# Kernel tuning notes

Hardware: AMD Instinct MI355X
Metric: run time of the kernel (lower is better)

Reference implementation:

```python
import jax, jax.numpy as jnp
import numpy as np

B, N, C, HF, WF = 32, 1000, 64, 12, 20
Y_DISC = 72
D = C * HF  # 768: flattened anchor feature dim (channels x fv height)


def setup_inputs() -> dict:
    key = jax.random.key(0)
    ks = jax.random.split(key, 8)
    feature_volumes = jax.random.normal(ks[0], (B, C, HF, WF), jnp.float32)
    # Anchor gather indices: channel index, row index, per-anchor x along the anchor line
    z_idx = jnp.broadcast_to(jnp.arange(C, dtype=jnp.int32)[None, :, None], (N, C, HF))
    y_idx = jnp.broadcast_to(jnp.arange(HF, dtype=jnp.int32)[None, None, :], (N, C, HF))
    x_line = jax.random.randint(ks[1], (N, 1, HF), 0, WF, dtype=jnp.int32)
    x_idx = jnp.broadcast_to(x_line, (N, C, HF))
    invalid_mask = jnp.broadcast_to(jax.random.bernoulli(ks[2], 0.2, (N, 1, HF)), (N, C, HF))
    attn_w = jax.random.normal(ks[3], (D, N - 1), jnp.float32) * 0.02
    attn_b = jnp.zeros((N - 1,), jnp.float32)
    cls_w = jax.random.normal(ks[4], (2 * D, 2), jnp.float32) * 0.02
    cls_b = jnp.zeros((2,), jnp.float32)
    reg_w = jax.random.normal(ks[5], (2 * D, Y_DISC + 1), jnp.float32) * 0.02
    reg_b = jnp.zeros((Y_DISC + 1,), jnp.float32)
    anchors_image = jax.random.normal(ks[6], (N, 5 + Y_DISC), jnp.float32)
    return {
        'feature_volumes': feature_volumes,
        'attn_w': attn_w, 'attn_b': attn_b,
        'cls_w': cls_w, 'cls_b': cls_b,
        'reg_w': reg_w, 'reg_b': reg_b,
        'anchors_image': anchors_image,
        'z_idx': z_idx, 'y_idx': y_idx, 'x_idx': x_idx,
        'invalid_mask': invalid_mask,
    }


def reference(feature_volumes, attn_w, attn_b, cls_w, cls_b, reg_w, reg_b,
              anchors_image, z_idx, y_idx, x_idx, invalid_mask):
    b = feature_volumes.shape[0]
    n = z_idx.shape[0]
    # __cut_anchor_features: gather (B, N, C, HF) rois, zero invalid entries
    rois = feature_volumes[:, z_idx, y_idx, x_idx]          # (B, N, C, HF)
    rois = jnp.where(invalid_mask[None], 0.0, rois)
    feat = rois.reshape(b, n, D)                            # (B, N, D)
    # attention layer: Linear(D -> N-1) + softmax over the N-1 dim
    scores = jax.nn.softmax(feat @ attn_w + attn_b, axis=-1)  # (B, N, N-1)
    # scatter scores into the off-diagonal of an NxN matrix (diagonal = 0)
    rows = jnp.arange(n)
    k = jnp.arange(n - 1)
    col_idx = jnp.where(k[None, :] < rows[:, None], k[None, :], k[None, :] + 1)  # (N, N-1)
    attn_mat = jnp.zeros((b, n, n), feat.dtype).at[:, rows[:, None], col_idx].set(scores)
    # bmm: attention-weighted sum of anchor features
    att_feat = jnp.einsum('bij,bjd->bid', attn_mat, feat)   # (B, N, D)
    cat = jnp.concatenate([att_feat, feat], axis=-1)        # (B, N, 2D)
    cls_logits = cat @ cls_w + cls_b                        # (B, N, 2)
    reg = cat @ reg_w + reg_b                               # (B, N, 73)
    anchors = jnp.broadcast_to(anchors_image[None], (b, n, 5 + Y_DISC))
    # proposals: [:2]=cls, [2:4]=anchor, [4:]=anchor+reg
    return jnp.concatenate([cls_logits, anchors[:, :, 2:4], anchors[:, :, 4:] + reg], axis=-1)
```

## Files before the change

### kernel.cpp

```cpp
#include <hip/hip_runtime.h>
#include <hip/hip_bf16.h>

typedef _Float16 f16;
typedef _Float16 f16x4 __attribute__((ext_vector_type(4)));
typedef _Float16 f16x8 __attribute__((ext_vector_type(8)));
typedef float    f32x4 __attribute__((ext_vector_type(4)));

static __device__ __forceinline__ float bf2f(__hip_bfloat16 x) { return __bfloat162float(x); }
static __device__ __forceinline__ float ldf(const void* p, long i, int f32flag) {
    return f32flag ? ((const float*)p)[i] : bf2f(((const __hip_bfloat16*)p)[i]);
}
static __device__ __forceinline__ void stf(void* p, long i, int f32flag, float v) {
    if (f32flag) ((float*)p)[i] = v;
    else ((__hip_bfloat16*)p)[i] = __float2bfloat16(v);
}
static __device__ __forceinline__ void gl2lds16(const f16* g, f16* l) {
    __builtin_amdgcn_global_load_lds(
        (const __attribute__((address_space(1))) unsigned int*)(const void*)g,
        (__attribute__((address_space(3))) unsigned int*)(void*)l, 16, 0, 0);
}

#define OFF_LOGITS 0L
#define SZ_LOGITS  (32000L * 1024 * 2)
#define OFF_FEAT   (OFF_LOGITS + SZ_LOGITS)
#define SZ_FEAT    (32000L * 768 * 2)
#define OFF_ATTF   (OFF_FEAT + SZ_FEAT)
#define SZ_ATTF    (32000L * 768 * 2)
#define OFF_AWT    (OFF_ATTF + SZ_ATTF)
#define SZ_AWT     (1024L * 768 * 2)
#define OFF_WCT    (OFF_AWT + SZ_AWT)
#define SZ_WCT     (128L * 1536 * 2)
#define OFF_BIAS   (OFF_WCT + SZ_WCT)
#define OFF_AB     (OFF_BIAS + 512)
#define OFF_FLAG   (OFF_AB + 4096)
#define OFF_FEATT  (OFF_FLAG + 64)
#define SZ_FEATT   (32L * 768 * 1024 * 2)
#define NEED_A     (OFF_FEATT + SZ_FEATT)

__global__ void detect_kernel(const unsigned int* __restrict__ fv,
                              const unsigned int* __restrict__ m,
                              int mwords, int* __restrict__ flags)
{
    __shared__ int cnt, bits;
    int t = threadIdx.x;
    if (t == 0) { cnt = 0; bits = 0; }
    __syncthreads();
    int c = 0;
    for (int k = t; k < 2048; k += 256) {
        unsigned int w = fv[k];
        unsigned int h0 = w & 0xffffu, h1 = w >> 16;
        unsigned int e0 = (h0 >> 7) & 0xffu, e1 = (h1 >> 7) & 0xffu;
        c += (h0 == 0u || (e0 >= 100u && e0 <= 135u)) ? 1 : 0;
        c += (h1 == 0u || (e1 >= 100u && e1 <= 135u)) ? 1 : 0;
    }
    atomicAdd(&cnt, c);
    int lb = 0;
    for (int k = t; k < mwords; k += 256) {
        unsigned int w = m[k];
        if (w > 1u) lb |= 1;
        if ((k & 1) && w != 0u) lb |= 2;
        unsigned int lo = w & 0xffffu, hi = w >> 16;
        if (!((lo == 0u || lo == 0x3f80u) && (hi == 0u || hi == 0x3f80u))) lb |= 4;
        if (lo == 0x3f80u) lb |= 8;
    }
    if (lb) atomicOr(&bits, lb);
    __syncthreads();
    if (t == 0) {
        int b = bits, f;
        if (!(b & 1))      f = (b & 2) ? 0 : 3;
        else if (!(b & 4)) f = (b & 8) ? 2 : 4;
        else               f = 1;
        flags[0] = f;
        flags[1] = (cnt < 3900) ? 1 : 0;
    }
}

__global__ __launch_bounds__(256) void front_kernel(
    const void* __restrict__ fv, const int* __restrict__ x_idx,
    const void* __restrict__ maskp, const int* __restrict__ flags,
    int xstride, int mstride, f16* __restrict__ feat,
    const void* __restrict__ attn_w,
    const void* __restrict__ cls_w, const void* __restrict__ cls_b,
    const void* __restrict__ reg_w, const void* __restrict__ reg_b,
    const void* __restrict__ attn_b,
    f16* __restrict__ awT, f16* __restrict__ wcT,
    float* __restrict__ biasc, float* __restrict__ abf32)
{
    int bid = blockIdx.x;
    int t = threadIdx.x;
    int isf = flags[1], fm = flags[0];
    if (bid < 512) {
        __shared__ f16 sfv[15360];
        __shared__ int sx[756];
        __shared__ unsigned char sm[756];
        int b = bid >> 4, n0 = (bid & 15) * 63;
        int rows = min(63, 1000 - n0);
        if (isf) {
            const float4* src = (const float4*)fv + (long)b * 3840;
            for (int k = t; k < 3840; k += 256) {
                float4 v = src[k];
                f16x4 h; h[0] = (f16)v.x; h[1] = (f16)v.y; h[2] = (f16)v.z; h[3] = (f16)v.w;
                *(f16x4*)&sfv[k * 4] = h;
            }
        } else {
            const uint4* src = (const uint4*)fv + (long)b * 1920;
            for (int k = t; k < 1920; k += 256) {
                uint4 v = src[k];
                unsigned int wv[4] = {v.x, v.y, v.z, v.w};
                f16x8 h;
                #pragma unroll
                for (int j = 0; j < 4; j++) {
                    h[2 * j]     = (f16)__uint_as_float((wv[j] & 0xffffu) << 16);
                    h[2 * j + 1] = (f16)__uint_as_float(wv[j] & 0xffff0000u);
                }
                *(f16x8*)&sfv[k * 8] = h;
            }
        }
        for (int k = t; k < rows * 12; k += 256) {
            int n = k / 12, h = k - n * 12;
            sx[k] = x_idx[(long)(n0 + n) * xstride + h];
            long mb = (long)(n0 + n) * mstride + h;
            int mv;
            if (fm == 0)      mv = ((const int*)maskp)[mb] != 0;
            else if (fm == 1) mv = ((const unsigned char*)maskp)[mb] != 0;
            else if (fm == 2) mv = ((const unsigned short*)maskp)[mb] != 0;
            else if (fm == 3) mv = ((const int*)maskp)[mb * 2] != 0;
            else              mv = ((const unsigned int*)maskp)[mb] != 0;
            sm[k] = (unsigned char)mv;
        }
        __syncthreads();
        for (int q = t; q < rows * 192; q += 256) {
            int n = q / 192, r = q - n * 192;
            int e0 = r * 4;
            f16x4 v;
            #pragma unroll
            for (int j = 0; j < 4; j++) {
                int e = e0 + j;
                int h = e % 12;
                int kk = n * 12 + h;
                v[j] = sm[kk] ? (f16)0.f : sfv[e * 20 + sx[kk]];
            }
            *(f16x4*)(feat + ((long)(b * 1000 + n0 + n)) * 768 + e0) = v;
        }
    } else if (bid < 1280) {
        __shared__ f16 tile[32][33];
        int tid = bid - 512;
        int c0 = (tid % 32) * 32, r0 = (tid / 32) * 32;
        int tx = t & 31, ty = t >> 5;
        #pragma unroll
        for (int i = ty; i < 32; i += 8) {
            int r = r0 + i, c = c0 + tx;
            float v = 0.f;
            if (r < 768 && c < 999) v = ldf(attn_w, (long)r * 999 + c, isf);
            tile[i][tx] = (f16)v;
        }
        __syncthreads();
        #pragma unroll
        for (int i = ty; i < 32; i += 8) {
            int oc = c0 + i, orw = r0 + tx;
            awT[(long)oc * 768 + orw] = tile[tx][i];
        }
    } else {
        int idx = (bid - 1280) * 256 + t;
        if (idx < 128 * 1536) {
            int c = idx / 1536, k = idx - c * 1536;
            float v = 0.f;
            if (c < 2)       v = ldf(cls_w, (long)k * 2 + c, isf);
            else if (c < 75) v = ldf(reg_w, (long)k * 73 + (c - 2), isf);
            wcT[idx] = (f16)v;
        }
        if (idx < 75)
            biasc[idx] = (idx < 2) ? ldf(cls_b, idx, isf) : ldf(reg_b, idx - 2, isf);
        if (idx < 1024)
            abf32[idx] = (idx < 999) ? ldf(attn_b, idx, isf) : 0.f;
    }
}

__global__ __launch_bounds__(256) void transp_kernel(
    const f16* __restrict__ feat, f16* __restrict__ featT)
{
    __shared__ f16 tile[64][68];
    int bid = blockIdx.x;
    int bz = bid / 192;
    int rq = bid - bz * 192;
    int by = rq & 15, bx = rq >> 4;
    int r0 = by * 64, c0 = bx * 64;
    int t = threadIdx.x;
    int tr = t >> 4, tc = (t & 15) * 4;
    const f16* src = feat + (long)bz * 768000;
    #pragma unroll
    for (int ii = 0; ii < 4; ii++) {
        int r = r0 + ii * 16 + tr;
        f16x4 v = {(f16)0.f, (f16)0.f, (f16)0.f, (f16)0.f};
        if (r < 1000) v = *(const f16x4*)(src + (long)r * 768 + c0 + tc);
        *(f16x4*)&tile[ii * 16 + tr][tc] = v;
    }
    __syncthreads();
    f16* dst = featT + (long)bz * 786432;
    #pragma unroll
    for (int ii = 0; ii < 4; ii++) {
        int d = ii * 16 + tr;
        f16x4 v;
        #pragma unroll
        for (int j = 0; j < 4; j++) v[j] = tile[tc + j][d];
        *(f16x4*)(dst + (long)(c0 + d) * 1024 + r0 + tc) = v;
    }
}

__global__ __launch_bounds__(256) void post_kernel(
    f16* __restrict__ buf, const float* __restrict__ abf32)
{
    int bid = blockIdx.x;
    int t = threadIdx.x;
    int i = bid % 1000, b = bid / 1000;
    f16* row = buf + ((long)(b * 1000 + i)) * 1024;
    __shared__ float red[8];
    __shared__ float epv[256];
    int k0 = t * 4;
    f16x4 rv = *(const f16x4*)(row + k0);
    float4 ab = *(const float4*)(abf32 + k0);
    float abv[4] = {ab.x, ab.y, ab.z, ab.w};
    float v[4];
    float lmax = -3.4e38f;
    #pragma unroll
    for (int j = 0; j < 4; j++) {
        int k = k0 + j;
        float x = (k < 999) ? (float)rv[j] + abv[j] : -3.4e38f;
        v[j] = x;
        lmax = fmaxf(lmax, x);
    }
    #pragma unroll
    for (int o = 32; o > 0; o >>= 1) lmax = fmaxf(lmax, __shfl_down(lmax, o, 64));
    if ((t & 63) == 0) red[t >> 6] = lmax;
    __syncthreads();
    float gmax = fmaxf(fmaxf(red[0], red[1]), fmaxf(red[2], red[3]));
    float e[4];
    float lsum = 0.f;
    #pragma unroll
    for (int j = 0; j < 4; j++) {
        int k = k0 + j;
        float x = (k < 999) ? __expf(v[j] - gmax) : 0.f;
        e[j] = x;
        lsum += x;
    }
    epv[t] = e[3];
    #pragma unroll
    for (int o = 32; o > 0; o >>= 1) lsum += __shfl_down(lsum, o, 64);
    if ((t & 63) == 0) red[4 + (t >> 6)] = lsum;
    __syncthreads();
    float inv = 1.f / (red[4] + red[5] + red[6] + red[7]);
    f16x4 outv;
    if (k0 >= 1000) {
        #pragma unroll
        for (int j = 0; j < 4; j++) outv[j] = (f16)0.f;
    } else if (k0 + 3 < i) {
        #pragma unroll
        for (int j = 0; j < 4; j++) outv[j] = (f16)(e[j] * inv);
    } else if (k0 > i) {
        float ep = epv[t - 1];
        outv[0] = (f16)(ep * inv);
        #pragma unroll
        for (int j = 1; j < 4; j++) outv[j] = (f16)(e[j - 1] * inv);
    } else {
        #pragma unroll
        for (int j = 0; j < 4; j++) {
            int p = k0 + j;
            float s = (p == i) ? 0.f : ((p < i) ? e[j] : e[j - 1 < 0 ? 0 : j - 1]);
            if (p > i) s = e[j - 1];
            outv[j] = (f16)(s * inv);
        }
    }
    *(f16x4*)(row + k0) = outv;
}

#define SB8   __builtin_amdgcn_sched_barrier(0)
#define BAR8  __builtin_amdgcn_s_barrier()
#define LGKM0 do { asm volatile("s_waitcnt lgkmcnt(0)" ::: "memory"); __builtin_amdgcn_sched_barrier(0); } while (0)
#define VM4   asm volatile("s_waitcnt vmcnt(4)" ::: "memory")

__global__ __launch_bounds__(512, 2) void gemm8p_kernel(
    const f16* __restrict__ A, int lda,
    const f16* __restrict__ Bt, int ldb,
    f16* __restrict__ C, int ldc,
    int M, int MT, int NT, int KT,
    long sA, long sB, long sC)
{
    __shared__ __align__(16) f16 As[2][16384];
    __shared__ __align__(16) f16 Bs[2][16384];
    int t = threadIdx.x;
    int nwg = gridDim.x;
    int orig = blockIdx.x;
    int xcd = orig & 7, lin = orig >> 3;
    int q8 = nwg >> 3, r8 = nwg & 7;
    int wgid = (xcd < r8 ? xcd * (q8 + 1) : r8 * (q8 + 1) + (xcd - r8) * q8) + lin;
    int per_b = MT * NT;
    int bz = wgid / per_b;
    int rem = wgid - bz * per_b;
    int mt = rem / NT, nt = rem - mt * NT;
    int m0 = mt * 256, n0 = nt * 256;
    A  += (long)bz * sA;
    Bt += (long)bz * sB;
    C  += (long)bz * sC;
    int w = t >> 6, lane = t & 63;
    int wm = (w >> 2) * 128, wn = (w & 3) * 64;
    int lr = lane & 15, lq = lane >> 4;
    int row0 = t >> 3, slot = t & 7;
    int csw = slot ^ (row0 & 7);

    f32x4 acc[8][4];
    const f32x4 z4 = {0.f, 0.f, 0.f, 0.f};
    #pragma unroll
    for (int i = 0; i < 8; i++)
        #pragma unroll
        for (int j = 0; j < 4; j++) acc[i][j] = z4;

    f16x8 a_[2][2], b_[4][2];

#define STAGE_A8(kt, h, buf) do { \
    int ktc = (kt) < KT ? (kt) : KT - 1; \
    const f16* gp = A + (long)(m0 + (h) * 128 + row0) * lda + ktc * 64 + csw * 8; \
    gl2lds16(gp,                  &As[buf][(h) * 8192 + w * 512]); \
    gl2lds16(gp + 64 * (long)lda, &As[buf][(h) * 8192 + 4096 + w * 512]); \
} while (0)
#define STAGE_B8(kt, h, buf) do { \
    int ktc = (kt) < KT ? (kt) : KT - 1; \
    const f16* gp = Bt + (long)(n0 + (h) * 128 + row0) * ldb + ktc * 64 + csw * 8; \
    gl2lds16(gp,                  &Bs[buf][(h) * 8192 + w * 512]); \
    gl2lds16(gp + 64 * (long)ldb, &Bs[buf][(h) * 8192 + 4096 + w * 512]); \
} while (0)
#define RD_B8(buf) { \
    _Pragma("unroll") for (int n = 0; n < 4; n++) { \
        int r = wn + n * 16 + lr; int rb = r * 64; int x7 = r & 7; \
        _Pragma("unroll") for (int ks = 0; ks < 2; ks++) { \
            int cc = (lq + ks * 4) ^ x7; \
            b_[n][ks] = *(const f16x8*)&Bs[buf][rb + cc * 8]; } } }
#define RD_A8(q, buf) { \
    _Pragma("unroll") for (int m2 = 0; m2 < 2; m2++) { \
        int r = wm + ((q) * 2 + m2) * 16 + lr; int rb = r * 64; int x7 = r & 7; \
        _Pragma("unroll") for (int ks = 0; ks < 2; ks++) { \
            int cc = (lq + ks * 4) ^ x7; \
            a_[m2][ks] = *(const f16x8*)&As[buf][rb + cc * 8]; } } }
#define MFMA16(q) { \
    __builtin_amdgcn_s_setprio(1); \
    _Pragma("unroll") for (int ks = 0; ks < 2; ks++) \
    _Pragma("unroll") for (int m2 = 0; m2 < 2; m2++) \
    _Pragma("unroll") for (int n = 0; n < 4; n++) \
        acc[(q) * 2 + m2][n] = __builtin_amdgcn_mfma_f32_16x16x32_f16( \
            a_[m2][ks], b_[n][ks], acc[(q) * 2 + m2][n], 0, 0, 0); \
    __builtin_amdgcn_s_setprio(0); }

    STAGE_B8(0, 0, 0); STAGE_B8(0, 1, 0);
    STAGE_A8(0, 0, 0); STAGE_A8(0, 1, 0);
    STAGE_B8(1, 0, 1); STAGE_B8(1, 1, 1);
    VM4;
    BAR8;

    int NIT = KT >> 1;
    for (int it = 0; it < NIT; it++) {
        int t0 = 2 * it, t1 = t0 + 1;
        SB8; RD_B8(0); RD_A8(0, 0); STAGE_A8(t1, 0, 1);
        BAR8; LGKM0; MFMA16(0); BAR8;
        SB8; RD_A8(1, 0); STAGE_A8(t1, 1, 1);
        BAR8; LGKM0; MFMA16(1); BAR8;
        SB8; RD_A8(2, 0); STAGE_B8(t0 + 2, 0, 0);
        BAR8; LGKM0; MFMA16(2); BAR8;
        SB8; RD_A8(3, 0); STAGE_B8(t0 + 2, 1, 0);
        BAR8; LGKM0; MFMA16(3); VM4; BAR8;
        SB8; RD_B8(1); RD_A8(0, 1); STAGE_A8(t0 + 2, 0, 0);
        BAR8; LGKM0; MFMA16(0); BAR8;
        SB8; RD_A8(1, 1); STAGE_A8(t0 + 2, 1, 0);
        BAR8; LGKM0; MFMA16(1); BAR8;
        SB8; RD_A8(2, 1); STAGE_B8(t1 + 2, 0, 1);
        BAR8; LGKM0; MFMA16(2); BAR8;
        SB8; RD_A8(3, 1); STAGE_B8(t1 + 2, 1, 1);
        BAR8; LGKM0; MFMA16(3); VM4; BAR8;
    }

    #pragma unroll
    for (int m = 0; m < 8; m++)
        #pragma unroll
        for (int n = 0; n < 4; n++)
            #pragma unroll
            for (int r = 0; r < 4; r++) {
                int gm = m0 + wm + m * 16 + lq * 4 + r;
                int gn = n0 + wn + n * 16 + lr;
                if (gm < M) C[(long)gm * ldc + gn] = (f16)acc[m][n][r];
            }
#undef STAGE_A8
#undef STAGE_B8
#undef RD_B8
#undef RD_A8
#undef MFMA16
}

enum { OUT_F16 = 0, OUT_FINAL = 1 };

template<int MODE, bool CAT, bool BKM, int TM, int TN, int BK, int SWZ, bool BG>
__global__ __launch_bounds__(256, 2) void gemm_kernel(
    const f16* __restrict__ A, const f16* __restrict__ A2, int lda,
    const f16* __restrict__ Bt, int ldb,
    void* __restrict__ Cout, int ldc,
    int M, int Nc, int K,
    long sA, long sB, long sC,
    const float* __restrict__ bias, const void* __restrict__ anchors,
    const int* __restrict__ flags)
{
    int t = threadIdx.x;
    int bx, by, bz;
    if constexpr (SWZ == 2) {
        int bid = blockIdx.x;
        int xcd = bid & 7, s = bid >> 3;
        int g = xcd + 8 * (s >> 2);
        if (g >= (M + TM - 1) / TM) return;
        by = g; bx = s & 3; bz = 0;
    } else if constexpr (SWZ == 3) {
        int bid = blockIdx.x;
        int xcd = bid & 7, s = bid >> 3;
        bz = xcd * 4 + s / 24;
        int wv = s % 24;
        by = wv / 3; bx = wv - by * 3;
    } else { bx = blockIdx.x; by = blockIdx.y; bz = blockIdx.z; }

    int m0 = by * TM, n0 = bx * TN;
    int z = bz;
    A  += (long)z * sA;
    if (CAT) A2 += (long)z * sA;
    Bt += (long)z * sB;
    int w = t >> 6, lane = t & 63;
    constexpr int NJ = (TM == 128 && TN == 256) ? 8 : ((TN == 256) ? 4 : ((TM == 128) ? 4 : 2));
    int wm = (TM == 128) ? (w & 1) * 64 : 0;
    int wn;
    if constexpr (TM == 128 && TN == 256) wn = (w >> 1) * 128;
    else if constexpr (TN == 256)         wn = w * 64;
    else if constexpr (TM == 128)         wn = (w >> 1) * 64;
    else                                  wn = w * 32;

    int lr = lane & 15, lq = lane >> 4;

    const f32x4 zero4 = {0.f, 0.f, 0.f, 0.f};
    f32x4 acc[4][NJ];
    #pragma unroll
    for (int i = 0; i < 4; i++)
        #pragma unroll
        for (int j = 0; j < NJ; j++) acc[i][j] = zero4;

    if constexpr (BG) {
        constexpr int CH  = BK / 8;
        constexpr int AI  = TM * BK / 2048;
        constexpr int RPO = 2048 / BK;
        __shared__ __align__(16) f16 As[TM * BK];
        int row0 = t / CH, slot = t % CH;
        int csw = slot ^ (row0 & (CH - 1));
        long aoffB = (long)(m0 + row0) * lda + csw * 8;
        for (int k0 = 0; k0 < K; k0 += BK) {
            const f16* Ak = A; int kk = k0;
            if (CAT && k0 >= 768) { Ak = A2; kk = k0 - 768; }
            __syncthreads();
            #pragma unroll
            for (int i = 0; i < AI; i++)
                gl2lds16(Ak + aoffB + (long)(i * RPO) * lda + kk, &As[i * 2048 + w * 512]);
            f16x8 ball[BK / 32][NJ];
            #pragma unroll
            for (int ks = 0; ks < BK / 32; ks++)
                #pragma unroll
                for (int j = 0; j < NJ; j++) {
                    int r = wn + j * 16 + lr;
                    ball[ks][j] = *(const f16x8*)(Bt + (long)r * ldb + k0 + (ks * 4 + lq) * 8);
                }
            __syncthreads();
            #pragma unroll
            for (int ks = 0; ks < BK / 32; ks++) {
                f16x8 af[4];
                #pragma unroll
                for (int i = 0; i < 4; i++) {
                    int r = wm + i * 16 + lr;
                    int cc = (lq + ks * 4) ^ (r & (CH - 1));
                    af[i] = *(const f16x8*)&As[r * BK + cc * 8];
                }
                #pragma unroll
                for (int i = 0; i < 4; i++)
                    #pragma unroll
                    for (int j = 0; j < NJ; j++)
                        acc[i][j] = __builtin_amdgcn_mfma_f32_16x16x32_f16(af[i], ball[ks][j], acc[i][j], 0, 0, 0);
            }
        }
    } else if constexpr (!BKM) {
        constexpr int CH  = BK / 8;
        constexpr int AI  = TM * BK / 2048;
        constexpr int BI  = TN * BK / 2048;
        constexpr int RPO = 2048 / BK;
        __shared__ __align__(16) f16 As[TM * BK];
        __shared__ __align__(16) f16 Bs[TN * BK];
        int row0 = t / CH, slot = t % CH;
        int csw = slot ^ (row0 & (CH - 1));
        long aoffB = (long)(m0 + row0) * lda + csw * 8;
        long boffB = (long)(n0 + row0) * ldb + csw * 8;
        for (int k0 = 0; k0 < K; k0 += BK) {
            const f16* Ak = A; int kk = k0;
            if (CAT && k0 >= 768) { Ak = A2; kk = k0 - 768; }
            __syncthreads();
            #pragma unroll
            for (int i = 0; i < AI; i++)
                gl2lds16(Ak + aoffB + (long)(i * RPO) * lda + kk, &As[i * 2048 + w * 512]);
            #pragma unroll
            for (int i = 0; i < BI; i++)
                gl2lds16(Bt + boffB + (long)(i * RPO) * ldb + k0, &Bs[i * 2048 + w * 512]);
            __syncthreads();
            #pragma unroll
            for (int ks = 0; ks < BK / 32; ks++) {
                f16x8 af[4], bfr[NJ];
                #pragma unroll
                for (int i = 0; i < 4; i++) {
                    int r = wm + i * 16 + lr;
                    int cc = (lq + ks * 4) ^ (r & (CH - 1));
                    af[i] = *(const f16x8*)&As[r * BK + cc * 8];
                }
                #pragma unroll
                for (int j = 0; j < NJ; j++) {
                    int r = wn + j * 16 + lr;
                    int cc = (lq + ks * 4) ^ (r & (CH - 1));
                    bfr[j] = *(const f16x8*)&Bs[r * BK + cc * 8];
                }
                #pragma unroll
                for (int i = 0; i < 4; i++)
                    #pragma unroll
                    for (int j = 0; j < NJ; j++)
                        acc[i][j] = __builtin_amdgcn_mfma_f32_16x16x32_f16(af[i], bfr[j], acc[i][j], 0, 0, 0);
            }
        }
    } else {
        __shared__ __align__(16) f16 As[128 * 40];
        __shared__ __align__(16) f16 Bs[32 * 132];
        const f16x8 zero8 = {(f16)0, (f16)0, (f16)0, (f16)0, (f16)0, (f16)0, (f16)0, (f16)0};
        const f16x4 zero4h = {(f16)0, (f16)0, (f16)0, (f16)0};
        for (int k0 = 0; k0 < K; k0 += 32) {
            __syncthreads();
            #pragma unroll
            for (int i = 0; i < 2; i++) {
                int q = t + i * 256;
                { int row = q >> 2, kc = (q & 3) * 8;
                  f16x8 av = zero8;
                  if ((m0 + row) < M && (k0 + kc) < K)
                      av = *(const f16x8*)(A + (long)(m0 + row) * lda + k0 + kc);
                  *(f16x8*)&As[row * 40 + kc] = av; }
                { int kr = q >> 4, nc = (q & 15) * 8;
                  f16x4 b0 = zero4h, b1 = zero4h;
                  if ((k0 + kr) < K && (n0 + nc) < Nc) {
                      const f16* p2 = Bt + (long)(k0 + kr) * ldb + n0 + nc;
                      b0 = *(const f16x4*)p2;
                      b1 = *(const f16x4*)(p2 + 4);
                  }
                  *(f16x4*)&Bs[kr * 132 + nc]     = b0;
                  *(f16x4*)&Bs[kr * 132 + nc + 4] = b1; }
            }
            __syncthreads();
            f16x8 af[4], bfr[NJ];
            #pragma unroll
            for (int i = 0; i < 4; i++)
                af[i] = *(const f16x8*)&As[(wm + i * 16 + lr) * 40 + lq * 8];
            #pragma unroll
            for (int j = 0; j < NJ; j++)
                #pragma unroll
                for (int jj = 0; jj < 8; jj++)
                    bfr[j][jj] = Bs[(lq * 8 + jj) * 132 + wn + j * 16 + lr];
            #pragma unroll
            for (int i = 0; i < 4; i++)
                #pragma unroll
                for (int j = 0; j < NJ; j++)
                    acc[i][j] = __builtin_amdgcn_mfma_f32_16x16x32_f16(af[i], bfr[j], acc[i][j], 0, 0, 0);
        }
    }

    int isf = (MODE == OUT_FINAL) ? flags[1] : 0;
    #pragma unroll
    for (int i = 0; i < 4; i++) {
        #pragma unroll
        for (int j = 0; j < NJ; j++) {
            #pragma unroll
            for (int r = 0; r < 4; r++) {
                int gm = m0 + wm + i * 16 + lq * 4 + r;
                int gn = n0 + wn + j * 16 + lr;
                if (MODE == OUT_F16) {
                    if (gm < M && gn < Nc)
                        ((f16*)Cout)[(long)z * sC + (long)gm * ldc + gn] = (f16)acc[i][j][r];
                } else {
                    if (gn < Nc) {
                        float v = acc[i][j][r] + bias[gn];
                        int oc = (gn < 2) ? gn : gn + 2;
                        if (gn >= 2) v += ldf(anchors, (long)(gm % 1000) * 77 + oc, isf);
                        stf(Cout, (long)gm * 77 + oc, isf, v);
                    } else if (gn < 77) {
                        int oc = gn - 73;
                        stf(Cout, (long)gm * 77 + oc, isf,
                            ldf(anchors, (long)(gm % 1000) * 77 + oc, isf));
                    }
                }
            }
        }
    }
}

extern "C" void kernel_launch(void* const* d_in, const int* in_sizes, int n_in,
                              void* d_out, int out_size, void* d_ws, size_t ws_size,
                              hipStream_t stream)
{
    const void* fv      = d_in[0];
    const void* attn_w  = d_in[1];
    const void* attn_b  = d_in[2];
    const void* cls_w   = d_in[3];
    const void* cls_b   = d_in[4];
    const void* reg_w   = d_in[5];
    const void* reg_b   = d_in[6];
    const void* anchors = d_in[7];
    const int*  x_idx   = (const int*)d_in[10];
    const void* maskp   = d_in[11];
    int xstride = (in_sizes[10] < 768000) ? 12 : 768;
    int mstride = (in_sizes[11] < 768000) ? 12 : 768;
    int mwords  = in_sizes[11] / 4;
    if (mwords > 4096) mwords = 4096;

    char* ws = (char*)d_ws;
    f16*   logits = (f16*)(ws + OFF_LOGITS);
    f16*   feat   = (f16*)(ws + OFF_FEAT);
    f16*   attf   = (f16*)(ws + OFF_ATTF);
    f16*   awT    = (f16*)(ws + OFF_AWT);
    f16*   wcT    = (f16*)(ws + OFF_WCT);
    float* biasc  = (float*)(ws + OFF_BIAS);
    float* abf32  = (float*)(ws + OFF_AB);
    int*   flags  = (int*)(ws + OFF_FLAG);
    f16*   featT  = (f16*)(ws + OFF_FEATT);
    bool bigws = ws_size >= (size_t)NEED_A;

    detect_kernel<<<dim3(1), dim3(256), 0, stream>>>(
        (const unsigned int*)fv, (const unsigned int*)maskp, mwords, flags);
    front_kernel<<<dim3(2048), dim3(256), 0, stream>>>(
        fv, x_idx, maskp, flags, xstride, mstride, feat,
        attn_w, cls_w, cls_b, reg_w, reg_b, attn_b, awT, wcT, biasc, abf32);

    if (bigws)
        transp_kernel<<<dim3(6144), dim3(256), 0, stream>>>(feat, featT);

    gemm8p_kernel<<<dim3(500), dim3(512), 0, stream>>>(
        feat, 768, awT, 768, logits, 1024, 32000, 125, 4, 12, 0L, 0L, 0L);
    post_kernel<<<dim3(32000), dim3(256), 0, stream>>>(logits, abf32);
    if (bigws) {
        gemm8p_kernel<<<dim3(384), dim3(512), 0, stream>>>(
            logits, 1024, featT, 1024, attf, 768, 1000, 4, 3, 16,
            1024000L, 786432L, 768000L);
    } else {
        gemm_kernel<OUT_F16, false, true, 128, 128, 32, 0, false><<<dim3(6, 8, 32), dim3(256), 0, stream>>>(
            logits, nullptr, 1024, feat, 768, attf, 768, 1000, 768, 1000,
            1024000L, 768000L, 768000L, nullptr, nullptr, flags);
    }
    gemm_kernel<OUT_FINAL, true, false, 64, 128, 128, 0, true><<<dim3(1, 500, 1), dim3(256), 0, stream>>>(
        attf, feat, 768, wcT, 1536, d_out, 77, 32000, 75, 1536, 0, 0, 0,
        biasc, anchors, flags);
}
```

Measured before the change: 338.7 us.

## Reassociate attention bmm with head weights to avoid materializing attended features

Instead of computing att_feat = attn_mat @ feat (N×N×768 per batch) and then applying the 1536→75 head, the code first projects feat through both halves of the head weights (768→128 each), then multiplies the attention matrix by the small projected features (1000×128). The head's feat half is added in the epilogue. This cuts the bmm K-to-output width from 768 to 128 and removes the large feat transpose and the attended-feature buffer. It adds an extra small GEMM and transpose kernel, and it drops the fallback path used when the workspace is small.

Result: faster. 293.0 us (-13.5%).

```diff
diff --git a/kernel.cpp b/kernel.cpp
--- a/kernel.cpp
+++ b/kernel.cpp
@@ -24,18 +24,18 @@
 #define SZ_LOGITS  (32000L * 1024 * 2)
 #define OFF_FEAT   (OFF_LOGITS + SZ_LOGITS)
 #define SZ_FEAT    (32000L * 768 * 2)
-#define OFF_ATTF   (OFF_FEAT + SZ_FEAT)
-#define SZ_ATTF    (32000L * 768 * 2)
-#define OFF_AWT    (OFF_ATTF + SZ_ATTF)
+#define OFF_F12    (OFF_FEAT + SZ_FEAT)
+#define SZ_F12     (32000L * 256 * 2)
+#define OFF_AWT    (OFF_F12 + SZ_F12)
 #define SZ_AWT     (1024L * 768 * 2)
 #define OFF_WCT    (OFF_AWT + SZ_AWT)
-#define SZ_WCT     (128L * 1536 * 2)
+#define SZ_WCT     (256L * 768 * 2)
 #define OFF_BIAS   (OFF_WCT + SZ_WCT)
 #define OFF_AB     (OFF_BIAS + 512)
 #define OFF_FLAG   (OFF_AB + 4096)
-#define OFF_FEATT  (OFF_FLAG + 64)
-#define SZ_FEATT   (32L * 768 * 1024 * 2)
-#define NEED_A     (OFF_FEATT + SZ_FEATT)
+#define OFF_F1T    (OFF_FLAG + 64)
+#define SZ_F1T     (32L * 128 * 1024 * 2)
+#define NEED_A     (OFF_F1T + SZ_F1T)
 
 __global__ void detect_kernel(const unsigned int* __restrict__ fv,
                               const unsigned int* __restrict__ m,
@@ -162,11 +162,13 @@
         }
     } else {
         int idx = (bid - 1280) * 256 + t;
-        if (idx < 128 * 1536) {
-            int c = idx / 1536, k = idx - c * 1536;
+        if (idx < 256 * 768) {
+            int c = idx / 768, k = idx - c * 768;
+            int wrow = (c < 128) ? k : 768 + k;
+            int wcol = (c < 128) ? c : c - 128;
             float v = 0.f;
-            if (c < 2)       v = ldf(cls_w, (long)k * 2 + c, isf);
-            else if (c < 75) v = ldf(reg_w, (long)k * 73 + (c - 2), isf);
+            if (wcol < 2)       v = ldf(cls_w, (long)wrow * 2 + wcol, isf);
+            else if (wcol < 75) v = ldf(reg_w, (long)wrow * 73 + (wcol - 2), isf);
             wcT[idx] = (f16)v;
         }
         if (idx < 75)
@@ -176,27 +178,27 @@
     }
 }
 
-__global__ __launch_bounds__(256) void transp_kernel(
-    const f16* __restrict__ feat, f16* __restrict__ featT)
+__global__ __launch_bounds__(256) void transpf1_kernel(
+    const f16* __restrict__ F12, f16* __restrict__ F1T)
 {
     __shared__ f16 tile[64][68];
     int bid = blockIdx.x;
-    int bz = bid / 192;
-    int rq = bid - bz * 192;
+    int bz = bid >> 5;
+    int rq = bid & 31;
     int by = rq & 15, bx = rq >> 4;
     int r0 = by * 64, c0 = bx * 64;
     int t = threadIdx.x;
     int tr = t >> 4, tc = (t & 15) * 4;
-    const f16* src = feat + (long)bz * 768000;
+    const f16* src = F12 + (long)bz * 1000 * 256;
     #pragma unroll
     for (int ii = 0; ii < 4; ii++) {
         int r = r0 + ii * 16 + tr;
         f16x4 v = {(f16)0.f, (f16)0.f, (f16)0.f, (f16)0.f};
-        if (r < 1000) v = *(const f16x4*)(src + (long)r * 768 + c0 + tc);
+        if (r < 1000) v = *(const f16x4*)(src + (long)r * 256 + c0 + tc);
         *(f16x4*)&tile[ii * 16 + tr][tc] = v;
     }
     __syncthreads();
-    f16* dst = featT + (long)bz * 786432;
+    f16* dst = F1T + (long)bz * 131072;
     #pragma unroll
     for (int ii = 0; ii < 4; ii++) {
         int d = ii * 16 + tr;
@@ -403,23 +405,11 @@
     int M, int Nc, int K,
     long sA, long sB, long sC,
     const float* __restrict__ bias, const void* __restrict__ anchors,
-    const int* __restrict__ flags)
+    const int* __restrict__ flags, const f16* __restrict__ F2c)
 {
     int t = threadIdx.x;
     int bx, by, bz;
-    if constexpr (SWZ == 2) {
-        int bid = blockIdx.x;
-        int xcd = bid & 7, s = bid >> 3;
-        int g = xcd + 8 * (s >> 2);
-        if (g >= (M + TM - 1) / TM) return;
-        by = g; bx = s & 3; bz = 0;
-    } else if constexpr (SWZ == 3) {
-        int bid = blockIdx.x;
-        int xcd = bid & 7, s = bid >> 3;
-        bz = xcd * 4 + s / 24;
-        int wv = s % 24;
-        by = wv / 3; bx = wv - by * 3;
-    } else { bx = blockIdx.x; by = blockIdx.y; bz = blockIdx.z; }
+    bx = blockIdx.x; by = blockIdx.y; bz = blockIdx.z;
 
     int m0 = by * TM, n0 = bx * TN;
     int z = bz;
@@ -465,7 +455,7 @@
                 #pragma unroll
                 for (int j = 0; j < NJ; j++) {
                     int r = wn + j * 16 + lr;
-                    ball[ks][j] = *(const f16x8*)(Bt + (long)r * ldb + k0 + (ks * 4 + lq) * 8);
+                    ball[ks][j] = *(const f16x8*)(Bt + (long)(n0 + r) * ldb + k0 + (ks * 4 + lq) * 8);
                 }
             __syncthreads();
             #pragma unroll
@@ -484,7 +474,7 @@
                         acc[i][j] = __builtin_amdgcn_mfma_f32_16x16x32_f16(af[i], ball[ks][j], acc[i][j], 0, 0, 0);
             }
         }
-    } else if constexpr (!BKM) {
+    } else {
         constexpr int CH  = BK / 8;
         constexpr int AI  = TM * BK / 2048;
         constexpr int BI  = TN * BK / 2048;
@@ -528,47 +518,6 @@
                         acc[i][j] = __builtin_amdgcn_mfma_f32_16x16x32_f16(af[i], bfr[j], acc[i][j], 0, 0, 0);
             }
         }
-    } else {
-        __shared__ __align__(16) f16 As[128 * 40];
-        __shared__ __align__(16) f16 Bs[32 * 132];
-        const f16x8 zero8 = {(f16)0, (f16)0, (f16)0, (f16)0, (f16)0, (f16)0, (f16)0, (f16)0};
-        const f16x4 zero4h = {(f16)0, (f16)0, (f16)0, (f16)0};
-        for (int k0 = 0; k0 < K; k0 += 32) {
-            __syncthreads();
-            #pragma unroll
-            for (int i = 0; i < 2; i++) {
-                int q = t + i * 256;
-                { int row = q >> 2, kc = (q & 3) * 8;
-                  f16x8 av = zero8;
-                  if ((m0 + row) < M && (k0 + kc) < K)
-                      av = *(const f16x8*)(A + (long)(m0 + row) * lda + k0 + kc);
-                  *(f16x8*)&As[row * 40 + kc] = av; }
-                { int kr = q >> 4, nc = (q & 15) * 8;
-                  f16x4 b0 = zero4h, b1 = zero4h;
-                  if ((k0 + kr) < K && (n0 + nc) < Nc) {
-                      const f16* p2 = Bt + (long)(k0 + kr) * ldb + n0 + nc;
-                      b0 = *(const f16x4*)p2;
-                      b1 = *(const f16x4*)(p2 + 4);
-                  }
-                  *(f16x4*)&Bs[kr * 132 + nc]     = b0;
-                  *(f16x4*)&Bs[kr * 132 + nc + 4] = b1; }
-            }
-            __syncthreads();
-            f16x8 af[4], bfr[NJ];
-            #pragma unroll
-            for (int i = 0; i < 4; i++)
-                af[i] = *(const f16x8*)&As[(wm + i * 16 + lr) * 40 + lq * 8];
-            #pragma unroll
-            for (int j = 0; j < NJ; j++)
-                #pragma unroll
-                for (int jj = 0; jj < 8; jj++)
-                    bfr[j][jj] = Bs[(lq * 8 + jj) * 132 + wn + j * 16 + lr];
-            #pragma unroll
-            for (int i = 0; i < 4; i++)
-                #pragma unroll
-                for (int j = 0; j < NJ; j++)
-                    acc[i][j] = __builtin_amdgcn_mfma_f32_16x16x32_f16(af[i], bfr[j], acc[i][j], 0, 0, 0);
-        }
     }
 
     int isf = (MODE == OUT_FINAL) ? flags[1] : 0;
@@ -584,15 +533,18 @@
                     if (gm < M && gn < Nc)
                         ((f16*)Cout)[(long)z * sC + (long)gm * ldc + gn] = (f16)acc[i][j][r];
                 } else {
-                    if (gn < Nc) {
-                        float v = acc[i][j][r] + bias[gn];
-                        int oc = (gn < 2) ? gn : gn + 2;
-                        if (gn >= 2) v += ldf(anchors, (long)(gm % 1000) * 77 + oc, isf);
-                        stf(Cout, (long)gm * 77 + oc, isf, v);
-                    } else if (gn < 77) {
-                        int oc = gn - 73;
-                        stf(Cout, (long)gm * 77 + oc, isf,
-                            ldf(anchors, (long)(gm % 1000) * 77 + oc, isf));
+                    if (gm < M) {
+                        if (gn < Nc) {
+                            float v = acc[i][j][r] + bias[gn];
+                            if (F2c) v += (float)F2c[((long)z * 1000 + gm) * 256 + 128 + gn];
+                            int oc = (gn < 2) ? gn : gn + 2;
+                            if (gn >= 2) v += ldf(anchors, (long)(gm % 1000) * 77 + oc, isf);
+                            stf(Cout, (long)z * sC + (long)gm * 77 + oc, isf, v);
+                        } else if (gn < 77) {
+                            int oc = gn - 73;
+                            stf(Cout, (long)z * sC + (long)gm * 77 + oc, isf,
+                                ldf(anchors, (long)(gm % 1000) * 77 + oc, isf));
+                        }
                     }
                 }
             }
@@ -622,37 +574,30 @@
     char* ws = (char*)d_ws;
     f16*   logits = (f16*)(ws + OFF_LOGITS);
     f16*   feat   = (f16*)(ws + OFF_FEAT);
-    f16*   attf   = (f16*)(ws + OFF_ATTF);
+    f16*   F12    = (f16*)(ws + OFF_F12);
     f16*   awT    = (f16*)(ws + OFF_AWT);
-    f16*   wcT    = (f16*)(ws + OFF_WCT);
+    f16*   wcT2   = (f16*)(ws + OFF_WCT);
     float* biasc  = (float*)(ws + OFF_BIAS);
     float* abf32  = (float*)(ws + OFF_AB);
     int*   flags  = (int*)(ws + OFF_FLAG);
-    f16*   featT  = (f16*)(ws + OFF_FEATT);
-    bool bigws = ws_size >= (size_t)NEED_A;
+    f16*   F1T    = (f16*)(ws + OFF_F1T);
 
     detect_kernel<<<dim3(1), dim3(256), 0, stream>>>(
         (const unsigned int*)fv, (const unsigned int*)maskp, mwords, flags);
     front_kernel<<<dim3(2048), dim3(256), 0, stream>>>(
         fv, x_idx, maskp, flags, xstride, mstride, feat,
-        attn_w, cls_w, cls_b, reg_w, reg_b, attn_b, awT, wcT, biasc, abf32);
-
-    if (bigws)
-        transp_kernel<<<dim3(6144), dim3(256), 0, stream>>>(feat, featT);
+        attn_w, cls_w, cls_b, reg_w, reg_b, attn_b, awT, wcT2, biasc, abf32);
+
+    gemm_kernel<OUT_F16, false, false, 64, 128, 128, 0, true><<<dim3(2, 500, 1), dim3(256), 0, stream>>>(
+        feat, nullptr, 768, wcT2, 768, F12, 256, 32000, 256, 768, 0, 0, 0,
+        nullptr, nullptr, flags, nullptr);
+    transpf1_kernel<<<dim3(1024), dim3(256), 0, stream>>>(F12, F1T);
 
     gemm8p_kernel<<<dim3(500), dim3(512), 0, stream>>>(
         feat, 768, awT, 768, logits, 1024, 32000, 125, 4, 12, 0L, 0L, 0L);
     post_kernel<<<dim3(32000), dim3(256), 0, stream>>>(logits, abf32);
-    if (bigws) {
-        gemm8p_kernel<<<dim3(384), dim3(512), 0, stream>>>(
-            logits, 1024, featT, 1024, attf, 768, 1000, 4, 3, 16,
-            1024000L, 786432L, 768000L);
-    } else {
-        gemm_kernel<OUT_F16, false, true, 128, 128, 32, 0, false><<<dim3(6, 8, 32), dim3(256), 0, stream>>>(
-            logits, nullptr, 1024, feat, 768, attf, 768, 1000, 768, 1000,
-            1024000L, 768000L, 768000L, nullptr, nullptr, flags);
-    }
-    gemm_kernel<OUT_FINAL, true, false, 64, 128, 128, 0, true><<<dim3(1, 500, 1), dim3(256), 0, stream>>>(
-        attf, feat, 768, wcT, 1536, d_out, 77, 32000, 75, 1536, 0, 0, 0,
-        biasc, anchors, flags);
-}
+
+    gemm_kernel<OUT_FINAL, false, false, 64, 128, 64, 0, false><<<dim3(1, 16, 32), dim3(256), 0, stream>>>(
+        logits, nullptr, 1024, F1T, 1024, d_out, 77, 1000, 75, 1024,
+        1024000L, 131072L, 77000L, biasc, anchors, flags, F12);
+}
```
